# Performance work log

Hardware: AMD Instinct MI355X
Metric: run time of the kernel (lower is better)

## Reference

```python
import jax, jax.numpy as jnp
import numpy as np

D_HEAD = 64  # per-head dim 'd' from init_kwargs


def layer_norm(x, g, b, eps=1e-5):
    m = x.mean(-1, keepdims=True)
    v = x.var(-1, keepdims=True)  # biased var, matches torch LayerNorm
    return (x - m) / jnp.sqrt(v + eps) * g + b


def setup_inputs() -> dict:
    key = jax.random.key(0)
    ks = jax.random.split(key, 16)
    F = 512
    B, T, N = 2, 8, 1024
    s = 1.0 / np.sqrt(F)
    u = lambda k, shape: jax.random.uniform(k, shape, jnp.float32, -s, s)
    return {
        "x": jax.random.normal(ks[0], (B, T, N, F), jnp.float32),
        "Wq": u(ks[1], (F, F)), "bq": u(ks[2], (F,)),
        "Wk": u(ks[3], (F, F)), "bk": u(ks[4], (F,)),
        "Wv": u(ks[5], (F, F)), "bv": u(ks[6], (F,)),
        "ln_g": jnp.ones((F,), jnp.float32), "ln_b": jnp.zeros((F,), jnp.float32),
        "W1": u(ks[7], (F, F)), "b1": u(ks[8], (F,)),
        "W2": u(ks[9], (F, F)), "b2": u(ks[10], (F,)),
        "lnff_g": jnp.ones((F,), jnp.float32), "lnff_b": jnp.zeros((F,), jnp.float32),
    }


def reference(x, Wq, bq, Wk, bk, Wv, bv, ln_g, ln_b, W1, b1, W2, b2, lnff_g, lnff_b):
    B, T, N, F = x.shape
    h = F // D_HEAD
    # q/k/v projections
    q = x @ Wq + bq
    k = x @ Wk + bk
    v = x @ Wv + bv
    # split last dim into heads (split+cat(dim=0) in torch == head axis here)
    qh = q.reshape(B, T, N, h, D_HEAD)
    kh = k.reshape(B, T, N, h, D_HEAD)
    vh = v.reshape(B, T, N, h, D_HEAD)
    # attention over node axis N per (batch, time, head)
    A = jnp.einsum('btqhd,btkhd->bthqk', qh, kh) / jnp.sqrt(jnp.asarray(D_HEAD, x.dtype))
    A = jax.nn.softmax(A, axis=-1)
    o = jnp.einsum('bthqk,btkhd->btqhd', A, vh).reshape(B, T, N, F)
    # residual + LN
    val = layer_norm(o + x, ln_g, ln_b)
    # FFN + final LN
    ff = jax.nn.relu(val @ W1 + b1) @ W2 + b2
    return layer_norm(ff, lnff_g, lnff_b)
```

## Files before the change

kernel.cpp:

```cpp
#include <hip/hip_runtime.h>
#include <hip/hip_bf16.h>

using bf16 = __hip_bfloat16;
typedef unsigned int u32x4 __attribute__((ext_vector_type(4)));
typedef float f32x4 __attribute__((ext_vector_type(4)));
typedef __bf16 bf16x8 __attribute__((ext_vector_type(8)));

#define DEVI __device__ __forceinline__

DEVI f32x4 mfma16(u32x4 a, u32x4 b, f32x4 c) {
    return __builtin_amdgcn_mfma_f32_16x16x32_bf16(
        __builtin_bit_cast(bf16x8, a), __builtin_bit_cast(bf16x8, b), c, 0, 0, 0);
}

struct bf8 { bf16 h[8]; };

DEVI u32x4 pack8(f32x4 lo, f32x4 hi) {
    bf8 t;
#pragma unroll
    for (int i = 0; i < 4; i++) {
        t.h[i] = __float2bfloat16(lo[i]);
        t.h[4 + i] = __float2bfloat16(hi[i]);
    }
    return __builtin_bit_cast(u32x4, t);
}

DEVI unsigned long long pk4(float a, float b, float c, float d) {
    union { unsigned long long u; bf16 h[4]; } t;
    t.h[0] = __float2bfloat16(a); t.h[1] = __float2bfloat16(b);
    t.h[2] = __float2bfloat16(c); t.h[3] = __float2bfloat16(d);
    return t.u;
}

DEVI unsigned trunc2(float a, float b) {
    return __builtin_amdgcn_perm(__builtin_bit_cast(unsigned, b),
                                 __builtin_bit_cast(unsigned, a), 0x07060302);
}

__global__ __launch_bounds__(256) void prep(
    const float* __restrict__ Wq, const float* __restrict__ Wk,
    const float* __restrict__ Wv, const float* __restrict__ W1,
    const float* __restrict__ W2, const float* __restrict__ x,
    bf16* __restrict__ WT, bf16* __restrict__ xb)
{
    int b = blockIdx.x;
    if (b < 5120) {
        int w = b >> 10;
        const float* src = (w == 0) ? Wq : (w == 1) ? Wk : (w == 2) ? Wv : (w == 3) ? W1 : W2;
        int idx = (b & 1023) * 256 + threadIdx.x;
        int n = idx >> 9, kk = idx & 511;
        WT[(size_t)w * 262144 + idx] = __float2bfloat16(src[kk * 512 + n]);
    } else {
        size_t i = ((size_t)(b - 5120) * 256 + threadIdx.x) * 8;
        f32x4 lo = *(const f32x4*)&x[i];
        f32x4 hi = *(const f32x4*)&x[i + 4];
        *(u32x4*)&xb[i] = pack8(lo, hi);
    }
}

#define GEMM_BODY(EPILOGUE)                                                          \
    constexpr int SP = 72;                                                           \
    __shared__ __align__(16) bf16 As[128 * SP];                                      \
    __shared__ __align__(16) bf16 Bs[128 * SP];                                      \
    const int tid = threadIdx.x;                                                     \
    const int lane = tid & 63, wave = tid >> 6;                                      \
    const int wm = (wave >> 1) * 64, wn = (wave & 1) * 64;                           \
    const int lm = lane & 15, lq = lane >> 4;                                        \
    const int sr = tid >> 3, sc = (tid & 7) * 8;             \
    const bf16* Ap = A + (size_t)(bm + sr) * 512 + sc;                               \
    const bf16* Bp = Bt + (size_t)(bn + sr) * 512 + sc;                              \
    f32x4 acc[4][4];                                                                 \
    _Pragma("unroll") for (int i = 0; i < 4; i++)                                    \
        _Pragma("unroll") for (int j = 0; j < 4; j++)                                \
            acc[i][j] = (f32x4){0.f, 0.f, 0.f, 0.f};                                 \
    u32x4 ar[4], br[4];                                                              \
    _Pragma("unroll") for (int p = 0; p < 4; p++) {                                  \
        ar[p] = *(const u32x4*)(Ap + (size_t)p * 32 * 512);                          \
        br[p] = *(const u32x4*)(Bp + (size_t)p * 32 * 512);                          \
    }                                                                                \
    for (int k0 = 0; k0 < 512; k0 += 64) {                                           \
        __syncthreads();                                                             \
        _Pragma("unroll") for (int p = 0; p < 4; p++) {                              \
            *(u32x4*)&As[(p * 32 + sr) * SP + sc] = ar[p];                           \
            *(u32x4*)&Bs[(p * 32 + sr) * SP + sc] = br[p];                           \
        }                                                                            \
        __syncthreads();                                                             \
        if (k0 < 448) {      \
            _Pragma("unroll") for (int p = 0; p < 4; p++) {                          \
                ar[p] = *(const u32x4*)(Ap + (size_t)p * 32 * 512 + k0 + 64);        \
                br[p] = *(const u32x4*)(Bp + (size_t)p * 32 * 512 + k0 + 64);        \
            }                                                                        \
        }                                                                            \
        _Pragma("unroll") for (int h = 0; h < 2; h++) {                              \
            u32x4 af[4], bfr[4];                                                     \
            _Pragma("unroll") for (int i = 0; i < 4; i++)                            \
                af[i] = *(const u32x4*)&As[(wm + i * 16 + lm) * SP + h * 32 + lq * 8]; \
            _Pragma("unroll") for (int j = 0; j < 4; j++)                            \
                bfr[j] = *(const u32x4*)&Bs[(wn + j * 16 + lm) * SP + h * 32 + lq * 8]; \
            EPILOGUE##_MMA                                                           \
        }                                                                            \
    }

#define SWAPPED_MMA                                                                  \
    _Pragma("unroll") for (int i = 0; i < 4; i++)                                    \
        _Pragma("unroll") for (int j = 0; j < 4; j++)                                \
            acc[i][j] = mfma16(bfr[j], af[i], acc[i][j]);
#define NORMAL_MMA                                                                   \
    _Pragma("unroll") for (int i = 0; i < 4; i++)                                    \
        _Pragma("unroll") for (int j = 0; j < 4; j++)                                \
            acc[i][j] = mfma16(af[i], bfr[j], acc[i][j]);

__global__ __launch_bounds__(256) void gemm_qkv(
    const bf16* __restrict__ A, const bf16* __restrict__ WT,
    const float* __restrict__ bqp, const float* __restrict__ bkp, const float* __restrict__ bvp,
    bf16* __restrict__ qb, bf16* __restrict__ kb, bf16* __restrict__ vT)
{
    const int wsel = blockIdx.y >> 2;
    const int bm = blockIdx.x * 128, bn = (blockIdx.y & 3) * 128;
    const bf16* Bt = WT + (size_t)wsel * 262144;
    const float* bias = (wsel == 0) ? bqp : (wsel == 1) ? bkp : bvp;

    if (wsel < 2) {
        GEMM_BODY(SWAPPED)
        const float scale = (wsel == 0) ? 0.18033688f : 1.0f;
        bf16* dst = (wsel == 0) ? qb : kb;
#pragma unroll
        for (int i = 0; i < 4; i++) {
#pragma unroll
            for (int j = 0; j < 4; j++) {
                int row = bm + wm + i * 16 + lm;
                int colb = bn + wn + j * 16 + lq * 4;
                f32x4 b4 = *(const f32x4*)&bias[colb];
                *(unsigned long long*)&dst[(size_t)row * 512 + colb] =
                    pk4((acc[i][j][0] + b4[0]) * scale, (acc[i][j][1] + b4[1]) * scale,
                        (acc[i][j][2] + b4[2]) * scale, (acc[i][j][3] + b4[3]) * scale);
            }
        }
    } else {
        GEMM_BODY(NORMAL)
#pragma unroll
        for (int i = 0; i < 4; i++) {
#pragma unroll
            for (int j = 0; j < 4; j++) {
                int col = bn + wn + j * 16 + lm;
                float bv = bias[col];
                int rowb = bm + wm + i * 16 + lq * 4;
                int btq = rowb >> 10, node = rowb & 1023;
                *(unsigned long long*)&vT[((size_t)((btq * 8 + (col >> 6)) * 64 + (col & 63))) * 1024 + node] =
                    pk4(acc[i][j][0] + bv, acc[i][j][1] + bv,
                        acc[i][j][2] + bv, acc[i][j][3] + bv);
            }
        }
    }
}

template <bool RELU>
__global__ __launch_bounds__(256) void gemm_bt(
    const bf16* __restrict__ A, const bf16* __restrict__ Bt,
    const float* __restrict__ bias, bf16* __restrict__ C)
{
    const int bm = blockIdx.x * 128, bn = blockIdx.y * 128;
    GEMM_BODY(SWAPPED)
#pragma unroll
    for (int i = 0; i < 4; i++) {
#pragma unroll
        for (int j = 0; j < 4; j++) {
            int row = bm + wm + i * 16 + lm;
            int colb = bn + wn + j * 16 + lq * 4;
            f32x4 b4 = *(const f32x4*)&bias[colb];
            float c0 = acc[i][j][0] + b4[0], c1 = acc[i][j][1] + b4[1];
            float c2 = acc[i][j][2] + b4[2], c3 = acc[i][j][3] + b4[3];
            if (RELU) {
                c0 = fmaxf(c0, 0.f); c1 = fmaxf(c1, 0.f);
                c2 = fmaxf(c2, 0.f); c3 = fmaxf(c3, 0.f);
            }
            *(unsigned long long*)&C[(size_t)row * 512 + colb] = pk4(c0, c1, c2, c3);
        }
    }
}

__global__ __launch_bounds__(256) void attn_kernel(
    const bf16* __restrict__ q, const bf16* __restrict__ k,
    const bf16* __restrict__ vT, float* __restrict__ o)
{
    constexpr int KP = 72;
    constexpr int VP = 72;
    __shared__ __align__(16) bf16 Ks[64 * KP];
    __shared__ __align__(16) bf16 Vs[64 * VP];
    __shared__ __align__(16) bf16 Ps[4][64 * VP];

    const int tid = threadIdx.x, lane = tid & 63, wave = tid >> 6;
    const int group = blockIdx.x;
    const int bt = group >> 3, hh = group & 7;
    const int lm = lane & 15, lq = lane >> 4;
    const int qrow0 = bt * 1024 + blockIdx.y * 256 + wave * 64;

    u32x4 qf[4][2];
#pragma unroll
    for (int tm = 0; tm < 4; tm++)
#pragma unroll
        for (int kk2 = 0; kk2 < 2; kk2++)
            qf[tm][kk2] = *(const u32x4*)&q[(size_t)(qrow0 + tm * 16 + lm) * 512 + hh * 64 + kk2 * 32 + lq * 8];

    const bf16* kbase = k + (size_t)(bt * 1024) * 512 + hh * 64;
    const bf16* vbase = vT + (size_t)group * 64 * 1024;
    bf16* Pw = Ps[wave];

    const int r0 = tid >> 3, e0 = (tid & 7) * 8;
    const int r1 = (256 + tid) >> 3, e1 = e0;

    f32x4 accO[4][4];
#pragma unroll
    for (int tm = 0; tm < 4; tm++)
#pragma unroll
        for (int tn = 0; tn < 4; tn++) accO[tm][tn] = (f32x4){0.f, 0.f, 0.f, 0.f};
    float part[4] = {0.f, 0.f, 0.f, 0.f};

    u32x4 kreg0 = *(const u32x4*)&kbase[(size_t)r0 * 512 + e0];
    u32x4 kreg1 = *(const u32x4*)&kbase[(size_t)r1 * 512 + e1];
    u32x4 vreg0 = *(const u32x4*)&vbase[(size_t)r0 * 1024 + e0];
    u32x4 vreg1 = *(const u32x4*)&vbase[(size_t)r1 * 1024 + e1];

    for (int kt = 0; kt < 16; kt++) {
        __syncthreads();
        *(u32x4*)&Ks[r0 * KP + e0] = kreg0;
        *(u32x4*)&Ks[r1 * KP + e1] = kreg1;
        *(u32x4*)&Vs[r0 * VP + e0] = vreg0;
        *(u32x4*)&Vs[r1 * VP + e1] = vreg1;
        __syncthreads();
        if (kt < 15) {
            const bf16* kn = kbase + (size_t)((kt + 1) * 64) * 512;
            const bf16* vn = vbase + (kt + 1) * 64;
            kreg0 = *(const u32x4*)&kn[(size_t)r0 * 512 + e0];
            kreg1 = *(const u32x4*)&kn[(size_t)r1 * 512 + e1];
            vreg0 = *(const u32x4*)&vn[(size_t)r0 * 1024 + e0];
            vreg1 = *(const u32x4*)&vn[(size_t)r1 * 1024 + e1];
        }

#pragma unroll
        for (int tk = 0; tk < 4; tk++) {
            u32x4 kf0 = *(const u32x4*)&Ks[(tk * 16 + lm) * KP + lq * 8];
            u32x4 kf1 = *(const u32x4*)&Ks[(tk * 16 + lm) * KP + 32 + lq * 8];
#pragma unroll
            for (int tm = 0; tm < 4; tm++) {
                f32x4 st = (f32x4){0.f, 0.f, 0.f, 0.f};
                st = mfma16(kf0, qf[tm][0], st);
                st = mfma16(kf1, qf[tm][1], st);
                float p0 = __builtin_amdgcn_exp2f(st[0]);
                float p1 = __builtin_amdgcn_exp2f(st[1]);
                float p2 = __builtin_amdgcn_exp2f(st[2]);
                float p3 = __builtin_amdgcn_exp2f(st[3]);
                part[tm] += (p0 + p1) + (p2 + p3);
                unsigned lo = trunc2(p0, p1), hi = trunc2(p2, p3);
                unsigned long long pk2 = ((unsigned long long)hi << 32) | lo;
                *(unsigned long long*)&Pw[(tm * 16 + lm) * VP + tk * 16 + lq * 4] = pk2;
            }
        }

#pragma unroll
        for (int kc = 0; kc < 2; kc++) {
            u32x4 pf[4], vf[4];
#pragma unroll
            for (int tm = 0; tm < 4; tm++)
                pf[tm] = *(const u32x4*)&Pw[(tm * 16 + lm) * VP + kc * 32 + lq * 8];
#pragma unroll
            for (int tn = 0; tn < 4; tn++)
                vf[tn] = *(const u32x4*)&Vs[(tn * 16 + lm) * VP + kc * 32 + lq * 8];
#pragma unroll
            for (int tm = 0; tm < 4; tm++)
#pragma unroll
                for (int tn = 0; tn < 4; tn++)
                    accO[tm][tn] = mfma16(pf[tm], vf[tn], accO[tm][tn]);
        }
    }

#pragma unroll
    for (int tm = 0; tm < 4; tm++) {
        part[tm] += __shfl_xor(part[tm], 16);
        part[tm] += __shfl_xor(part[tm], 32);
    }
#pragma unroll
    for (int tm = 0; tm < 4; tm++)
#pragma unroll
        for (int r = 0; r < 4; r++) {
            float l = __shfl(part[tm], lq * 4 + r);
            float linv = 1.0f / l;
#pragma unroll
            for (int tn = 0; tn < 4; tn++) {
                int row = qrow0 + tm * 16 + lq * 4 + r;
                int col = hh * 64 + tn * 16 + lm;
                o[(size_t)row * 512 + col] = accO[tm][tn][r] * linv;
            }
        }
}

template <bool AF32, bool RES, bool OF32>
__global__ __launch_bounds__(256) void ln_kernel(
    const void* __restrict__ a, const float* __restrict__ res,
    const float* __restrict__ g, const float* __restrict__ bb, void* __restrict__ out)
{
    int row = blockIdx.x * 4 + (threadIdx.x >> 6);
    int lane = threadIdx.x & 63;
    size_t base = (size_t)row * 512 + lane * 8;
    int cbase = lane * 8;

    float x8[8];
    if (AF32) {
        const float* af = (const float*)a;
        f32x4 lo = *(const f32x4*)&af[base];
        f32x4 hi = *(const f32x4*)&af[base + 4];
#pragma unroll
        for (int i = 0; i < 4; i++) { x8[i] = lo[i]; x8[4 + i] = hi[i]; }
    } else {
        bf8 av = __builtin_bit_cast(bf8, *(const u32x4*)&((const bf16*)a)[base]);
#pragma unroll
        for (int i = 0; i < 8; i++) x8[i] = __bfloat162float(av.h[i]);
    }
    if (RES) {
        f32x4 lo = *(const f32x4*)&res[base];
        f32x4 hi = *(const f32x4*)&res[base + 4];
#pragma unroll
        for (int i = 0; i < 4; i++) { x8[i] += lo[i]; x8[4 + i] += hi[i]; }
    }

    float s = 0.f, s2 = 0.f;
#pragma unroll
    for (int i = 0; i < 8; i++) { s += x8[i]; s2 += x8[i] * x8[i]; }
#pragma unroll
    for (int off = 1; off < 64; off <<= 1) {
        s += __shfl_xor(s, off);
        s2 += __shfl_xor(s2, off);
    }
    float mean = s * (1.f / 512.f);
    float var = s2 * (1.f / 512.f) - mean * mean;
    float rstd = rsqrtf(var + 1e-5f);

    f32x4 g0 = *(const f32x4*)&g[cbase], g1 = *(const f32x4*)&g[cbase + 4];
    f32x4 b0 = *(const f32x4*)&bb[cbase], b1v = *(const f32x4*)&bb[cbase + 4];
    float y[8];
#pragma unroll
    for (int i = 0; i < 4; i++) {
        y[i] = (x8[i] - mean) * rstd * g0[i] + b0[i];
        y[4 + i] = (x8[4 + i] - mean) * rstd * g1[i] + b1v[i];
    }
    if (OF32) {
        float* op = (float*)out;
        *(f32x4*)&op[base] = (f32x4){y[0], y[1], y[2], y[3]};
        *(f32x4*)&op[base + 4] = (f32x4){y[4], y[5], y[6], y[7]};
    } else {
        bf8 ov;
#pragma unroll
        for (int i = 0; i < 8; i++) ov.h[i] = __float2bfloat16(y[i]);
        *(u32x4*)&((bf16*)out)[base] = __builtin_bit_cast(u32x4, ov);
    }
}

extern "C" void kernel_launch(void* const* d_in, const int* in_sizes, int n_in,
                              void* d_out, int out_size, void* d_ws, size_t ws_size,
                              hipStream_t stream)
{
    const float* x    = (const float*)d_in[0];
    const float* Wq   = (const float*)d_in[1];
    const float* bq   = (const float*)d_in[2];
    const float* Wk   = (const float*)d_in[3];
    const float* bk   = (const float*)d_in[4];
    const float* Wv   = (const float*)d_in[5];
    const float* bv   = (const float*)d_in[6];
    const float* ln_g = (const float*)d_in[7];
    const float* ln_b = (const float*)d_in[8];
    const float* W1   = (const float*)d_in[9];
    const float* b1   = (const float*)d_in[10];
    const float* W2   = (const float*)d_in[11];
    const float* b2   = (const float*)d_in[12];
    const float* lnffg = (const float*)d_in[13];
    const float* lnffb = (const float*)d_in[14];
    float* out = (float*)d_out;

    bf16* ws = (bf16*)d_ws;
    bf16* WT = ws;
    bf16* qb = ws + 5 * 262144;
    bf16* kb = qb + 8388608;
    bf16* vT = kb + 8388608;
    bf16* vl = qb;
    bf16* f1 = kb;
    bf16* f2 = vT;
    bf16* xb = (bf16*)d_out;

    prep<<<9216, 256, 0, stream>>>(Wq, Wk, Wv, W1, W2, x, WT, xb);

    gemm_qkv<<<dim3(128, 12), 256, 0, stream>>>(xb, WT, bq, bk, bv, qb, kb, vT);

    attn_kernel<<<dim3(128, 4), 256, 0, stream>>>(qb, kb, vT, out);

    ln_kernel<true, true, false><<<4096, 256, 0, stream>>>(out, x, ln_g, ln_b, vl);

    dim3 gg(128, 4);
    gemm_bt<true> <<<gg, 256, 0, stream>>>(vl, WT + 3 * 262144, b1, f1);
    gemm_bt<false><<<gg, 256, 0, stream>>>(f1, WT + 4 * 262144, b2, f2);

    ln_kernel<false, false, true><<<4096, 256, 0, stream>>>(f2, nullptr, lnffg, lnffb, out);
}
```

Baseline: 261.4 us.

## Keep attention probabilities in registers via permuted V layout, halve rows per wave

```diff
diff --git a/kernel.cpp b/kernel.cpp
--- a/kernel.cpp
+++ b/kernel.cpp
@@ -146,7 +146,9 @@
                 float bv = bias[col];
                 int rowb = bm + wm + i * 16 + lq * 4;
                 int btq = rowb >> 10, node = rowb & 1023;
-                *(unsigned long long*)&vT[((size_t)((btq * 8 + (col >> 6)) * 64 + (col & 63))) * 1024 + node] =
+                int u = node & 31;
+                int nodeP = (node & ~31) | (((u >> 2) & 3) << 3) | (((u >> 4) & 1) << 2);
+                *(unsigned long long*)&vT[((size_t)((btq * 8 + (col >> 6)) * 64 + (col & 63))) * 1024 + nodeP] =
                     pk4(acc[i][j][0] + bv, acc[i][j][1] + bv,
                         acc[i][j][2] + bv, acc[i][j][3] + bv);
             }
@@ -179,7 +181,7 @@
     }
 }
 
-__global__ __launch_bounds__(256) void attn_kernel(
+__global__ __launch_bounds__(256, 4) void attn_kernel(
     const bf16* __restrict__ q, const bf16* __restrict__ k,
     const bf16* __restrict__ vT, float* __restrict__ o)
 {
@@ -187,34 +189,32 @@
     constexpr int VP = 72;
     __shared__ __align__(16) bf16 Ks[64 * KP];
     __shared__ __align__(16) bf16 Vs[64 * VP];
-    __shared__ __align__(16) bf16 Ps[4][64 * VP];
 
     const int tid = threadIdx.x, lane = tid & 63, wave = tid >> 6;
     const int group = blockIdx.x;
     const int bt = group >> 3, hh = group & 7;
     const int lm = lane & 15, lq = lane >> 4;
-    const int qrow0 = bt * 1024 + blockIdx.y * 256 + wave * 64;
-
-    u32x4 qf[4][2];
-#pragma unroll
-    for (int tm = 0; tm < 4; tm++)
+    const int qrow0 = bt * 1024 + blockIdx.y * 128 + wave * 32;
+
+    u32x4 qf[2][2];
+#pragma unroll
+    for (int tm = 0; tm < 2; tm++)
 #pragma unroll
         for (int kk2 = 0; kk2 < 2; kk2++)
             qf[tm][kk2] = *(const u32x4*)&q[(size_t)(qrow0 + tm * 16 + lm) * 512 + hh * 64 + kk2 * 32 + lq * 8];
 
     const bf16* kbase = k + (size_t)(bt * 1024) * 512 + hh * 64;
     const bf16* vbase = vT + (size_t)group * 64 * 1024;
-    bf16* Pw = Ps[wave];
 
     const int r0 = tid >> 3, e0 = (tid & 7) * 8;
     const int r1 = (256 + tid) >> 3, e1 = e0;
 
-    f32x4 accO[4][4];
-#pragma unroll
-    for (int tm = 0; tm < 4; tm++)
-#pragma unroll
-        for (int tn = 0; tn < 4; tn++) accO[tm][tn] = (f32x4){0.f, 0.f, 0.f, 0.f};
-    float part[4] = {0.f, 0.f, 0.f, 0.f};
+    f32x4 accO[4][2];
+#pragma unroll
+    for (int md = 0; md < 4; md++)
+#pragma unroll
+        for (int tm = 0; tm < 2; tm++) accO[md][tm] = (f32x4){0.f, 0.f, 0.f, 0.f};
+    float part[2] = {0.f, 0.f};
 
     u32x4 kreg0 = *(const u32x4*)&kbase[(size_t)r0 * 512 + e0];
     u32x4 kreg1 = *(const u32x4*)&kbase[(size_t)r1 * 512 + e1];
@@ -238,60 +238,55 @@
         }
 
 #pragma unroll
-        for (int tk = 0; tk < 4; tk++) {
-            u32x4 kf0 = *(const u32x4*)&Ks[(tk * 16 + lm) * KP + lq * 8];
-            u32x4 kf1 = *(const u32x4*)&Ks[(tk * 16 + lm) * KP + 32 + lq * 8];
-#pragma unroll
-            for (int tm = 0; tm < 4; tm++) {
-                f32x4 st = (f32x4){0.f, 0.f, 0.f, 0.f};
-                st = mfma16(kf0, qf[tm][0], st);
-                st = mfma16(kf1, qf[tm][1], st);
-                float p0 = __builtin_amdgcn_exp2f(st[0]);
-                float p1 = __builtin_amdgcn_exp2f(st[1]);
-                float p2 = __builtin_amdgcn_exp2f(st[2]);
-                float p3 = __builtin_amdgcn_exp2f(st[3]);
-                part[tm] += (p0 + p1) + (p2 + p3);
-                unsigned lo = trunc2(p0, p1), hi = trunc2(p2, p3);
-                unsigned long long pk2 = ((unsigned long long)hi << 32) | lo;
-                *(unsigned long long*)&Pw[(tm * 16 + lm) * VP + tk * 16 + lq * 4] = pk2;
-            }
-        }
-
-#pragma unroll
         for (int kc = 0; kc < 2; kc++) {
-            u32x4 pf[4], vf[4];
-#pragma unroll
-            for (int tm = 0; tm < 4; tm++)
-                pf[tm] = *(const u32x4*)&Pw[(tm * 16 + lm) * VP + kc * 32 + lq * 8];
-#pragma unroll
-            for (int tn = 0; tn < 4; tn++)
-                vf[tn] = *(const u32x4*)&Vs[(tn * 16 + lm) * VP + kc * 32 + lq * 8];
-#pragma unroll
-            for (int tm = 0; tm < 4; tm++)
-#pragma unroll
-                for (int tn = 0; tn < 4; tn++)
-                    accO[tm][tn] = mfma16(pf[tm], vf[tn], accO[tm][tn]);
-        }
-    }
-
-#pragma unroll
-    for (int tm = 0; tm < 4; tm++) {
+            const int t0 = kc * 2;
+            u32x4 kf00 = *(const u32x4*)&Ks[(t0 * 16 + lm) * KP + lq * 8];
+            u32x4 kf01 = *(const u32x4*)&Ks[(t0 * 16 + lm) * KP + 32 + lq * 8];
+            u32x4 kf10 = *(const u32x4*)&Ks[((t0 + 1) * 16 + lm) * KP + lq * 8];
+            u32x4 kf11 = *(const u32x4*)&Ks[((t0 + 1) * 16 + lm) * KP + 32 + lq * 8];
+            u32x4 pw[2];
+#pragma unroll
+            for (int tm = 0; tm < 2; tm++) {
+                f32x4 s0 = (f32x4){0.f, 0.f, 0.f, 0.f};
+                s0 = mfma16(kf00, qf[tm][0], s0);
+                s0 = mfma16(kf01, qf[tm][1], s0);
+                f32x4 s1 = (f32x4){0.f, 0.f, 0.f, 0.f};
+                s1 = mfma16(kf10, qf[tm][0], s1);
+                s1 = mfma16(kf11, qf[tm][1], s1);
+                float p0 = __builtin_amdgcn_exp2f(s0[0]);
+                float p1 = __builtin_amdgcn_exp2f(s0[1]);
+                float p2 = __builtin_amdgcn_exp2f(s0[2]);
+                float p3 = __builtin_amdgcn_exp2f(s0[3]);
+                float p4 = __builtin_amdgcn_exp2f(s1[0]);
+                float p5 = __builtin_amdgcn_exp2f(s1[1]);
+                float p6 = __builtin_amdgcn_exp2f(s1[2]);
+                float p7 = __builtin_amdgcn_exp2f(s1[3]);
+                part[tm] += ((p0 + p1) + (p2 + p3)) + ((p4 + p5) + (p6 + p7));
+                pw[tm] = (u32x4){trunc2(p0, p1), trunc2(p2, p3),
+                                 trunc2(p4, p5), trunc2(p6, p7)};
+            }
+#pragma unroll
+            for (int md = 0; md < 4; md++) {
+                u32x4 vf = *(const u32x4*)&Vs[(md * 16 + lm) * VP + kc * 32 + lq * 8];
+                accO[md][0] = mfma16(vf, pw[0], accO[md][0]);
+                accO[md][1] = mfma16(vf, pw[1], accO[md][1]);
+            }
+        }
+    }
+
+#pragma unroll
+    for (int tm = 0; tm < 2; tm++) {
         part[tm] += __shfl_xor(part[tm], 16);
         part[tm] += __shfl_xor(part[tm], 32);
-    }
-#pragma unroll
-    for (int tm = 0; tm < 4; tm++)
-#pragma unroll
-        for (int r = 0; r < 4; r++) {
-            float l = __shfl(part[tm], lq * 4 + r);
-            float linv = 1.0f / l;
-#pragma unroll
-            for (int tn = 0; tn < 4; tn++) {
-                int row = qrow0 + tm * 16 + lq * 4 + r;
-                int col = hh * 64 + tn * 16 + lm;
-                o[(size_t)row * 512 + col] = accO[tm][tn][r] * linv;
-            }
-        }
+        float linv = 1.0f / part[tm];
+#pragma unroll
+        for (int md = 0; md < 4; md++) {
+            f32x4 r;
+#pragma unroll
+            for (int i = 0; i < 4; i++) r[i] = accO[md][tm][i] * linv;
+            *(f32x4*)&o[(size_t)(qrow0 + tm * 16 + lm) * 512 + hh * 64 + md * 16 + lq * 4] = r;
+        }
+    }
 }
 
 template <bool AF32, bool RES, bool OF32>
@@ -390,7 +385,7 @@
 
     gemm_qkv<<<dim3(128, 12), 256, 0, stream>>>(xb, WT, bq, bk, bv, qb, kb, vT);
 
-    attn_kernel<<<dim3(128, 4), 256, 0, stream>>>(qb, kb, vT, out);
+    attn_kernel<<<dim3(128, 8), 256, 0, stream>>>(qb, kb, vT, out);
 
     ln_kernel<true, true, false><<<4096, 256, 0, stream>>>(out, x, ln_g, ln_b, vl);
 
```

Measured after the change: 251.3 us. -3.9%, faster.
